# Kernel optimization log

Measured on AMD Instinct MI355X. Metric: run time of the kernel, lower is better.

The kernel has to match this reference:

```python
import jax, jax.numpy as jnp
from jax import lax
import numpy as np

NUM_HEADS = 8
ALPHA = 4.0  # spikingjelly default Sigmoid surrogate alpha
TAU = 2.0
BN_EPS = 1e-5

@jax.custom_vjp
def spike(x):
    # Heaviside(v - v_th) with sigmoid surrogate gradient
    return (x >= 0).astype(x.dtype)

def _spike_fwd(x):
    return spike(x), x

def _spike_bwd(x, g):
    sg = jax.nn.sigmoid(ALPHA * x)
    return (g * ALPHA * sg * (1.0 - sg),)

spike.defvjp(_spike_fwd, _spike_bwd)

def lif(x_seq, v_threshold=1.0):
    """Multi-step LIF, tau=2, hard reset to v_reset=0, detach_reset=True.
    x_seq: (T, ...) -> spikes (T, ...)."""
    def step(v, xt):
        h = v + (xt - v) / TAU
        s = spike(h - v_threshold)
        v_next = h * (1.0 - lax.stop_gradient(s))  # detach_reset hard reset
        return v_next, s
    _, s_seq = lax.scan(step, jnp.zeros_like(x_seq[0]), x_seq)
    return s_seq

def bn1d(x, gamma, beta, mean, var):
    # x: (T,B,C,N), normalize over channel dim C (eval-mode BatchNorm1d)
    inv = gamma / jnp.sqrt(var + BN_EPS)
    return x * inv[:, None] + (beta - mean * inv)[:, None]

def setup_inputs() -> dict:
    key = jax.random.key(0)
    ks = jax.random.split(key, 8)
    T, B, C, H, W = 4, 16, 384, 32, 32
    N = H * W
    Dh = C // NUM_HEADS
    x = jax.random.normal(ks[0], (T, B, C, H, W), dtype=jnp.float32)
    attn_k = jax.random.randint(ks[1], (T, B, NUM_HEADS, Dh, N), 0, 2).astype(jnp.bool_)
    attn_v = jax.random.randint(ks[2], (T, B, NUM_HEADS, Dh, N), 0, 2).astype(jnp.bool_)
    wq = jax.random.normal(ks[3], (C, C), dtype=jnp.float32) * 0.02
    wp = jax.random.normal(ks[4], (C, C), dtype=jnp.float32) * 0.02
    bp = jnp.zeros((C,), dtype=jnp.float32)
    return {
        'x': x, 'attn_k': attn_k, 'attn_v': attn_v,
        'wq': wq,
        'q_gamma': jnp.ones((C,), jnp.float32), 'q_beta': jnp.zeros((C,), jnp.float32),
        'q_mean': jnp.zeros((C,), jnp.float32), 'q_var': jnp.ones((C,), jnp.float32),
        'wp': wp, 'bp': bp,
        'p_gamma': jnp.ones((C,), jnp.float32), 'p_beta': jnp.zeros((C,), jnp.float32),
        'p_mean': jnp.zeros((C,), jnp.float32), 'p_var': jnp.ones((C,), jnp.float32),
    }

def reference(x, attn_k, attn_v, wq, q_gamma, q_beta, q_mean, q_var,
              wp, bp, p_gamma, p_beta, p_mean, p_var):
    T, B, C, H, W = x.shape
    N = H * W
    Dh = C // NUM_HEADS
    xs = lif(x).reshape(T, B, C, N)                      # shortcut_lif + flatten(3)
    q = jnp.einsum('oc,tbcn->tbon', wq, xs)              # q_conv (1x1, no bias)
    q = bn1d(q, q_gamma, q_beta, q_mean, q_var)          # q_bn
    q = lif(q)                                           # q_lif
    q = q.reshape(T, B, NUM_HEADS, Dh, N)
    kv = jnp.logical_and(attn_k, attn_v).astype(q.dtype) # attn_k & attn_v
    out = (q * kv).reshape(T, B, C, N)                   # elementwise 'attention'
    out = jnp.einsum('oc,tbcn->tbon', wp, out) + bp[:, None]  # proj_conv (bias)
    out = bn1d(out, p_gamma, p_beta, p_mean, p_var)      # proj_bn
    return out.reshape(T, B, C, H, W)
```

## Files before the change

kernel.cpp:

```cpp
#include <hip/hip_runtime.h>
#include <cstdint>

#define CN (384*1024)
#define BCN (16*CN)
#define EPS 1e-5f

typedef float f32x2 __attribute__((ext_vector_type(2)));
typedef float f32x4 __attribute__((ext_vector_type(4)));

#define WPT_OFF   0u
#define WQB_OFF   589824u
#define QINV_OFF  1179648u
#define QOFF_OFF  (QINV_OFF + 1536u)
#define PINV_OFF  (QINV_OFF + 3072u)
#define POFF_OFF  (QINV_OFF + 4608u)
#define C0_OFF    (QINV_OFF + 6144u)
#define LCNT2_OFF 1187840u
#define XM_OFF    1310720u
#define XMT_OFF   4456448u
#define LISTS2_OFF 7602176u
#define MST_OFF   XM_OFF

__global__ __launch_bounds__(256) void k01_lif_prep(const float* __restrict__ x,
                                                    const float* __restrict__ wq,
                                                    const float* __restrict__ wp,
                                                    const float* __restrict__ qg,
                                                    const float* __restrict__ qb,
                                                    const float* __restrict__ qm,
                                                    const float* __restrict__ qv,
                                                    const float* __restrict__ pg,
                                                    const float* __restrict__ pb,
                                                    const float* __restrict__ pm,
                                                    const float* __restrict__ pv,
                                                    const float* __restrict__ bp,
                                                    unsigned long long* __restrict__ xm,
                                                    char* __restrict__ ws) {
    if (blockIdx.x < 24576) {
        int wid  = (blockIdx.x * 256 + threadIdx.x) >> 6;
        int lane = threadIdx.x & 63;
        int c = wid % 384;
        int g = (wid / 384) & 15;
        int b = wid / (384 * 16);
        const float* xp = x + (size_t)b * CN + (size_t)c * 1024 + g * 64 + lane;
        float v = 0.f;
        #pragma unroll
        for (int t = 0; t < 4; ++t) {
            float xv = xp[(size_t)t * BCN];
            float h = v + (xv - v) * 0.5f;
            bool s = (h >= 1.0f);
            unsigned long long m = __ballot(s);
            v = s ? 0.f : h;
            if (lane == 0) xm[(((size_t)t * 16 + b) * 16 + g) * 384 + c] = m;
        }
        return;
    }
    int bid = blockIdx.x - 24576;
    if (bid < 576) {
        int i = bid * 256 + threadIdx.x;
        int c = i / 384, o = i % 384;
        ((float*)(ws + WPT_OFF))[c * 384 + o] = wp[o * 384 + c];
    } else if (bid < 1154) {
        int j = (bid - 576) * 256 + threadIdx.x;
        if (j >= 147840) return;
        int r = j / 384, o = j % 384;
        unsigned short v = 0;
        if (r < 384) {
            unsigned u = __float_as_uint(wq[o * 384 + r]);
            v = (unsigned short)((u + 0x7fffu + ((u >> 16) & 1u)) >> 16);
        }
        ((unsigned short*)(ws + WQB_OFF))[j] = v;
    } else {
        for (int i = threadIdx.x; i < 384; i += 256) {
            float qi = qg[i] / sqrtf(qv[i] + EPS);
            ((float*)(ws + QINV_OFF))[i] = qi;
            ((float*)(ws + QOFF_OFF))[i] = qb[i] - qm[i] * qi;
            float pi = pg[i] / sqrtf(pv[i] + EPS);
            float po = pb[i] - pm[i] * pi;
            ((float*)(ws + PINV_OFF))[i] = pi;
            ((float*)(ws + POFF_OFF))[i] = po;
            ((float*)(ws + C0_OFF))[i] = bp[i] * pi + po;
        }
    }
}

__global__ __launch_bounds__(256) void k1bc(const unsigned long long* __restrict__ xm,
                                            unsigned long long* __restrict__ xmT,
                                            unsigned short* __restrict__ lists2,
                                            unsigned char* __restrict__ lcnt2) {
    int wid  = (blockIdx.x * 256 + threadIdx.x) >> 6;
    int lane = threadIdx.x & 63;
    int g  = wid & 15;
    int tb = wid >> 4;
    unsigned long long T[6];
    #pragma unroll
    for (int cg = 0; cg < 6; ++cg) {
        unsigned long long W = xm[((size_t)tb * 16 + g) * 384 + cg * 64 + lane];
        unsigned long long colw = 0ull;
        #pragma unroll
        for (int k = 0; k < 64; ++k) {
            unsigned long long bk = __ballot((W >> k) & 1ull);
            if (lane == k) colw = bk;
        }
        T[cg] = colw;
    }
    const int n   = g * 64 + lane;
    const size_t col = ((size_t)tb << 10) + n;
    #pragma unroll
    for (int cg = 0; cg < 6; ++cg) xmT[col * 6 + cg] = T[cg];
    const int blockid = (tb & 15) * 64 + (n >> 4);
    const int un = (n & 15) * 4 + (tb >> 4);
    unsigned short* lp = lists2 + ((size_t)blockid * 64 + un) * 24;
    int k = 0;
    #pragma unroll
    for (int cg = 0; cg < 6; ++cg) {
        unsigned long long m = T[cg];
        while (m) {
            int j = __builtin_ctzll(m);
            m &= m - 1;
            if (k < 24) lp[k] = (unsigned short)((cg * 64 + j) * 3);
            ++k;
        }
    }
    int kk = k > 24 ? 24 : k;
    for (int i = kk; i < 24; ++i) lp[i] = 1152;
    lcnt2[(size_t)blockid * 64 + un] =
        (k > 24) ? 0xFF : (unsigned char)((k + 7) >> 3);
}

#define BLO(w) __uint_as_float((w) << 16)
#define BHI(w) __uint_as_float((w) & 0xFFFF0000u)
#define PK(w)  ((f32x2){BLO(w), BHI(w)})
#define RL(v, l) ((unsigned)__builtin_amdgcn_readlane((int)(v), (l)))

#define GROW8(W0, W1, W2, W3) do {                                                \
    uint3 d0_ = *(const uint3*)(wqc + ((size_t)((W0) & 0xffffu) << 8) + voff);    \
    uint3 d1_ = *(const uint3*)(wqc + ((size_t)((W0) >> 16) << 8) + voff);        \
    uint3 d2_ = *(const uint3*)(wqc + ((size_t)((W1) & 0xffffu) << 8) + voff);    \
    uint3 d3_ = *(const uint3*)(wqc + ((size_t)((W1) >> 16) << 8) + voff);        \
    uint3 d4_ = *(const uint3*)(wqc + ((size_t)((W2) & 0xffffu) << 8) + voff);    \
    uint3 d5_ = *(const uint3*)(wqc + ((size_t)((W2) >> 16) << 8) + voff);        \
    uint3 d6_ = *(const uint3*)(wqc + ((size_t)((W3) & 0xffffu) << 8) + voff);    \
    uint3 d7_ = *(const uint3*)(wqc + ((size_t)((W3) >> 16) << 8) + voff);        \
    s0 += ((PK(d0_.x) + PK(d1_.x)) + (PK(d2_.x) + PK(d3_.x)))                     \
        + ((PK(d4_.x) + PK(d5_.x)) + (PK(d6_.x) + PK(d7_.x)));                    \
    s1 += ((PK(d0_.y) + PK(d1_.y)) + (PK(d2_.y) + PK(d3_.y)))                     \
        + ((PK(d4_.y) + PK(d5_.y)) + (PK(d6_.y) + PK(d7_.y)));                    \
    s2 += ((PK(d0_.z) + PK(d1_.z)) + (PK(d2_.z) + PK(d3_.z)))                     \
        + ((PK(d4_.z) + PK(d5_.z)) + (PK(d6_.z) + PK(d7_.z)));                    \
} while (0)

__global__ __launch_bounds__(512) void k2_qpath(const char* __restrict__ wqc,
                                                const float* __restrict__ qinv_,
                                                const float* __restrict__ qoff_,
                                                const unsigned short* __restrict__ lists2,
                                                const unsigned char* __restrict__ lcnt2,
                                                const unsigned long long* __restrict__ xmT,
                                                const unsigned char* __restrict__ ak,
                                                const unsigned char* __restrict__ av,
                                                const float* __restrict__ c0,
                                                unsigned long long* __restrict__ msT,
                                                float* __restrict__ out) {
    const int tid  = threadIdx.x;
    const int lane = tid & 63;
    const int w    = tid >> 6;
    const int nt   = blockIdx.x & 63;
    const int b    = blockIdx.x >> 6;
    const int voff = lane * 12;

    const char* lb = (const char*)lists2 + (size_t)blockIdx.x * 3072 + lane * 48;
    const uint4 L0 = *(const uint4*)lb;
    const uint4 L1 = *(const uint4*)(lb + 16);
    const uint4 L2 = *(const uint4*)(lb + 32);
    const unsigned lcv = *(const unsigned*)((const char*)lcnt2
                          + (size_t)blockIdx.x * 64 + (lane & 15) * 4);

    float qi[6], qo[6];
    #pragma unroll
    for (int e = 0; e < 6; ++e) {
        qi[e] = qinv_[lane * 6 + e];
        qo[e] = qoff_[lane * 6 + e];
    }

    #pragma unroll
    for (int i = 0; i < 2; ++i) {
        const int nl = w * 2 + i;
        const int n  = nt * 16 + nl;
        const unsigned lcw = RL(lcv, nl);
        float v[6] = {0.f, 0.f, 0.f, 0.f, 0.f, 0.f};
        #pragma unroll
        for (int t = 0; t < 4; ++t) {
            const int un = nl * 4 + t;
            const unsigned r_ = (lcw >> (8 * t)) & 0xffu;
            f32x2 s0 = {0.f, 0.f}, s1 = {0.f, 0.f}, s2 = {0.f, 0.f};
            {
                const unsigned Wa = RL(L0.x, un), Wb = RL(L0.y, un);
                const unsigned Wc = RL(L0.z, un), Wd = RL(L0.w, un);
                const unsigned We = RL(L1.x, un), Wf = RL(L1.y, un);
                const unsigned Wg = RL(L1.z, un), Wh = RL(L1.w, un);
                GROW8(Wa, Wb, Wc, Wd);
                GROW8(We, Wf, Wg, Wh);
            }
            if (r_ == 3u) {
                const unsigned Wa = RL(L2.x, un), Wb = RL(L2.y, un);
                const unsigned Wc = RL(L2.z, un), Wd = RL(L2.w, un);
                GROW8(Wa, Wb, Wc, Wd);
            }
            if (r_ == 0xffu) {
                const int colf = ((t * 16 + b) << 10) + n;
                const unsigned long long* mp = xmT + (size_t)colf * 6;
                s0 = (f32x2){0.f, 0.f}; s1 = (f32x2){0.f, 0.f}; s2 = (f32x2){0.f, 0.f};
                #pragma unroll
                for (int cg = 0; cg < 6; ++cg) {
                    unsigned long long mm = mp[cg];
                    while (mm) {
                        int j = __builtin_ctzll(mm);
                        mm &= mm - 1;
                        uint3 dd = *(const uint3*)(wqc + (size_t)(cg * 64 + j) * 768 + voff);
                        s0 += PK(dd.x); s1 += PK(dd.y); s2 += PK(dd.z);
                    }
                }
            }
            const int col = ((t * 16 + b) << 10) + n;
            const float val[6] = {s0.x, s0.y, s1.x, s1.y, s2.x, s2.y};
            bool sp[6];
            #pragma unroll
            for (int e = 0; e < 6; ++e) {
                float q = val[e] * qi[e] + qo[e];
                float h = 0.5f * (v[e] + q);
                bool s = (h >= 1.0f);
                v[e] = s ? 0.f : h;
                if (s) {
                    size_t ix = ((size_t)((t * 16 + b) * 384 + lane * 6 + e) << 10) + n;
                    s = (ak[ix] != 0) && (av[ix] != 0);
                }
                sp[e] = s;
            }
            unsigned long long B0 = __ballot(sp[0]);
            unsigned long long B1 = __ballot(sp[1]);
            unsigned long long B2 = __ballot(sp[2]);
            unsigned long long B3 = __ballot(sp[3]);
            unsigned long long B4 = __ballot(sp[4]);
            unsigned long long B5 = __ballot(sp[5]);
            unsigned long long sel = lane == 0 ? B0 : lane == 1 ? B1 : lane == 2 ? B2
                                   : lane == 3 ? B3 : lane == 4 ? B4 : B5;
            if (lane < 6) msT[(size_t)col * 6 + lane] = sel;
        }
    }

    {
        float cv[3];
        #pragma unroll
        for (int k = 0; k < 3; ++k) cv[k] = c0[(tid + k * 512) >> 2];
        #pragma unroll
        for (int t = 0; t < 4; ++t) {
            f32x4* base4 = (f32x4*)out + (size_t)(t * 16 + b) * 384 * 256 + nt * 4;
            #pragma unroll
            for (int k = 0; k < 3; ++k) {
                int i2 = tid + k * 512;
                int o = i2 >> 2, n4 = i2 & 3;
                float vv = cv[k];
                __builtin_nontemporal_store((f32x4){vv, vv, vv, vv},
                                            base4 + (size_t)o * 256 + n4);
            }
        }
    }
}

__global__ __launch_bounds__(384) void k3_proj(const float* __restrict__ wpT,
                                               const float* __restrict__ pinv_,
                                               const float* __restrict__ poff_,
                                               const float* __restrict__ bp,
                                               const unsigned long long* __restrict__ msT,
                                               float* __restrict__ out) {
    __shared__ unsigned int wflag[6];
    const int tid = threadIdx.x;
    const int bid = blockIdx.x;
    const int g = bid & 15, b = (bid >> 4) & 15, t = bid >> 8;
    const unsigned long long* mbase = msT + ((size_t)(t * 16 + b) * 1024 + g * 64) * 6;
    unsigned long long m = mbase[tid];
    unsigned long long anyb = __ballot(m != 0ull);
    if ((tid & 63) == 0) wflag[tid >> 6] = (anyb != 0ull) ? 1u : 0u;
    __syncthreads();
    unsigned int any = wflag[0] | wflag[1] | wflag[2] | wflag[3] | wflag[4] | wflag[5];
    if (!any) return;

    size_t obase = (size_t)(t * 16 + b) * 384;
    float pi = pinv_[tid], po = poff_[tid], bb = bp[tid];
    for (int nl = 0; nl < 64; ++nl) {
        float acc = 0.f;
        #pragma unroll
        for (int u = 0; u < 6; ++u) {
            unsigned long long mm = mbase[nl * 6 + u];
            while (mm) {
                int j = __builtin_ctzll(mm);
                mm &= mm - 1;
                int row = j * 6 + u;
                acc += wpT[(size_t)row * 384 + tid];
            }
        }
        out[(obase + tid) * 1024 + g * 64 + nl] = (acc + bb) * pi + po;
    }
}

extern "C" void kernel_launch(void* const* d_in, const int* in_sizes, int n_in,
                              void* d_out, int out_size, void* d_ws, size_t ws_size,
                              hipStream_t stream) {
    const float* x  = (const float*)d_in[0];
    const unsigned char* ak = (const unsigned char*)d_in[1];
    const unsigned char* av = (const unsigned char*)d_in[2];
    const float* wq = (const float*)d_in[3];
    const float* qg = (const float*)d_in[4];
    const float* qb = (const float*)d_in[5];
    const float* qm = (const float*)d_in[6];
    const float* qv = (const float*)d_in[7];
    const float* wp = (const float*)d_in[8];
    const float* bp = (const float*)d_in[9];
    const float* pg = (const float*)d_in[10];
    const float* pb = (const float*)d_in[11];
    const float* pm = (const float*)d_in[12];
    const float* pv = (const float*)d_in[13];
    char* ws = (char*)d_ws;
    float* out = (float*)d_out;

    hipLaunchKernelGGL(k01_lif_prep, dim3(25731), dim3(256), 0, stream,
                       x, wq, wp, qg, qb, qm, qv, pg, pb, pm, pv, bp,
                       (unsigned long long*)(ws + XM_OFF), ws);
    hipLaunchKernelGGL(k1bc, dim3(256), dim3(256), 0, stream,
                       (const unsigned long long*)(ws + XM_OFF),
                       (unsigned long long*)(ws + XMT_OFF),
                       (unsigned short*)(ws + LISTS2_OFF),
                       (unsigned char*)(ws + LCNT2_OFF));
    hipLaunchKernelGGL(k2_qpath, dim3(1024), dim3(512), 0, stream,
                       (const char*)(ws + WQB_OFF),
                       (const float*)(ws + QINV_OFF), (const float*)(ws + QOFF_OFF),
                       (const unsigned short*)(ws + LISTS2_OFF),
                       (const unsigned char*)(ws + LCNT2_OFF),
                       (const unsigned long long*)(ws + XMT_OFF), ak, av,
                       (const float*)(ws + C0_OFF),
                       (unsigned long long*)(ws + MST_OFF), out);
    hipLaunchKernelGGL(k3_proj, dim3(1024), dim3(384), 0, stream,
                       (const float*)(ws + WPT_OFF), (const float*)(ws + PINV_OFF),
                       (const float*)(ws + POFF_OFF), bp,
                       (const unsigned long long*)(ws + MST_OFF), out);
}
```

Measured before the change: 93.98 us.

## Skip Q-path columns whose LIF membrane provably cannot reach threshold

Computes a per-input-channel max |bf16 weight| and global max BN scale/offset in the prep kernel. k1bc uses them to build, for each (t,n) column, a quantized upper bound on |q| from the active spike list. k2 runs that bound through the LIF recurrence and skips the whole gather-sum for columns that can never spike, writing zero masks instead. This is a sound, conservative bound, so results stay exact. It costs extra prep work and per-column bound bookkeeping, and it only pays off if enough columns have sparse inputs.

```diff
diff --git a/kernel.cpp b/kernel.cpp
--- a/kernel.cpp
+++ b/kernel.cpp
@@ -16,9 +16,12 @@
 #define POFF_OFF  (QINV_OFF + 4608u)
 #define C0_OFF    (QINV_OFF + 6144u)
 #define LCNT2_OFF 1187840u
+#define ROWMAX_OFF 1253376u
+#define MAXQ_OFF  1254912u
 #define XM_OFF    1310720u
 #define XMT_OFF   4456448u
 #define LISTS2_OFF 7602176u
+#define ABND_OFF  10747904u
 #define MST_OFF   XM_OFF
 
 __global__ __launch_bounds__(256) void k01_lif_prep(const float* __restrict__ x,
@@ -69,24 +72,63 @@
             v = (unsigned short)((u + 0x7fffu + ((u >> 16) & 1u)) >> 16);
         }
         ((unsigned short*)(ws + WQB_OFF))[j] = v;
-    } else {
+    } else if (bid == 1154) {
+        __shared__ float smi[256], smo[256];
+        float mi = 0.f, mo = 0.f;
         for (int i = threadIdx.x; i < 384; i += 256) {
             float qi = qg[i] / sqrtf(qv[i] + EPS);
             ((float*)(ws + QINV_OFF))[i] = qi;
-            ((float*)(ws + QOFF_OFF))[i] = qb[i] - qm[i] * qi;
+            float qov = qb[i] - qm[i] * qi;
+            ((float*)(ws + QOFF_OFF))[i] = qov;
             float pi = pg[i] / sqrtf(pv[i] + EPS);
             float po = pb[i] - pm[i] * pi;
             ((float*)(ws + PINV_OFF))[i] = pi;
             ((float*)(ws + POFF_OFF))[i] = po;
             ((float*)(ws + C0_OFF))[i] = bp[i] * pi + po;
+            mi = fmaxf(mi, fabsf(qi));
+            mo = fmaxf(mo, fabsf(qov));
+        }
+        smi[threadIdx.x] = mi; smo[threadIdx.x] = mo;
+        __syncthreads();
+        for (int s = 128; s > 0; s >>= 1) {
+            if (threadIdx.x < s) {
+                smi[threadIdx.x] = fmaxf(smi[threadIdx.x], smi[threadIdx.x + s]);
+                smo[threadIdx.x] = fmaxf(smo[threadIdx.x], smo[threadIdx.x + s]);
+            }
+            __syncthreads();
+        }
+        if (threadIdx.x == 0) {
+            ((float*)(ws + MAXQ_OFF))[0] = smi[0];
+            ((float*)(ws + MAXQ_OFF))[1] = smo[0];
+        }
+    } else {
+        __shared__ float sm[256];
+        int rblk = bid - 1155;
+        int row = rblk * 64 + (threadIdx.x >> 2);
+        int qd  = threadIdx.x & 3;
+        float m = 0.f;
+        for (int o = qd * 96; o < qd * 96 + 96; ++o) {
+            unsigned u = __float_as_uint(wq[(size_t)o * 384 + row]);
+            unsigned bbits = (u + 0x7fffu + ((u >> 16) & 1u)) >> 16;
+            m = fmaxf(m, __uint_as_float((bbits & 0x7fffu) << 16));
+        }
+        sm[threadIdx.x] = m;
+        __syncthreads();
+        if (qd == 0) {
+            float r0 = fmaxf(fmaxf(sm[threadIdx.x], sm[threadIdx.x + 1]),
+                             fmaxf(sm[threadIdx.x + 2], sm[threadIdx.x + 3]));
+            ((float*)(ws + ROWMAX_OFF))[row] = r0;
         }
     }
 }
 
 __global__ __launch_bounds__(256) void k1bc(const unsigned long long* __restrict__ xm,
+                                            const float* __restrict__ rowmaxp,
+                                            const float* __restrict__ maxqp,
                                             unsigned long long* __restrict__ xmT,
                                             unsigned short* __restrict__ lists2,
-                                            unsigned char* __restrict__ lcnt2) {
+                                            unsigned char* __restrict__ lcnt2,
+                                            unsigned char* __restrict__ abnd) {
     int wid  = (blockIdx.x * 256 + threadIdx.x) >> 6;
     int lane = threadIdx.x & 63;
     int g  = wid & 15;
@@ -111,12 +153,14 @@
     const int un = (n & 15) * 4 + (tb >> 4);
     unsigned short* lp = lists2 + ((size_t)blockid * 64 + un) * 24;
     int k = 0;
+    float S = 0.f;
     #pragma unroll
     for (int cg = 0; cg < 6; ++cg) {
         unsigned long long m = T[cg];
         while (m) {
             int j = __builtin_ctzll(m);
             m &= m - 1;
+            S += rowmaxp[cg * 64 + j];
             if (k < 24) lp[k] = (unsigned short)((cg * 64 + j) * 3);
             ++k;
         }
@@ -125,6 +169,9 @@
     for (int i = kk; i < 24; ++i) lp[i] = 1152;
     lcnt2[(size_t)blockid * 64 + un] =
         (k > 24) ? 0xFF : (unsigned char)((k + 7) >> 3);
+    float A = maxqp[0] * S + maxqp[1];
+    int aq = (int)ceilf(A * 64.f);
+    abnd[(size_t)blockid * 64 + un] = (unsigned char)(aq > 255 ? 255 : (aq < 0 ? 0 : aq));
 }
 
 #define BLO(w) __uint_as_float((w) << 16)
@@ -154,6 +201,7 @@
                                                 const float* __restrict__ qoff_,
                                                 const unsigned short* __restrict__ lists2,
                                                 const unsigned char* __restrict__ lcnt2,
+                                                const unsigned char* __restrict__ abnd,
                                                 const unsigned long long* __restrict__ xmT,
                                                 const unsigned char* __restrict__ ak,
                                                 const unsigned char* __restrict__ av,
@@ -173,6 +221,8 @@
     const uint4 L2 = *(const uint4*)(lb + 32);
     const unsigned lcv = *(const unsigned*)((const char*)lcnt2
                           + (size_t)blockIdx.x * 64 + (lane & 15) * 4);
+    const unsigned abv = *(const unsigned*)((const char*)abnd
+                          + (size_t)blockIdx.x * 64 + (lane & 15) * 4);
 
     float qi[6], qo[6];
     #pragma unroll
@@ -185,6 +235,23 @@
     for (int i = 0; i < 2; ++i) {
         const int nl = w * 2 + i;
         const int n  = nt * 16 + nl;
+        const unsigned abw = RL(abv, nl);
+        float hb = 0.f;
+        bool skip = true;
+        #pragma unroll
+        for (int t = 0; t < 4; ++t) {
+            float A = (float)((abw >> (8 * t)) & 0xffu) * 0.015625f + 0.015625f;
+            hb = 0.5f * (hb + A);
+            skip = skip && (hb < 1.0f);
+        }
+        if (skip) {
+            if (lane < 6) {
+                #pragma unroll
+                for (int t = 0; t < 4; ++t)
+                    msT[(size_t)(((t * 16 + b) << 10) + n) * 6 + lane] = 0ull;
+            }
+            continue;
+        }
         const unsigned lcw = RL(lcv, nl);
         float v[6] = {0.f, 0.f, 0.f, 0.f, 0.f, 0.f};
         #pragma unroll
@@ -322,19 +389,23 @@
     char* ws = (char*)d_ws;
     float* out = (float*)d_out;
 
-    hipLaunchKernelGGL(k01_lif_prep, dim3(25731), dim3(256), 0, stream,
+    hipLaunchKernelGGL(k01_lif_prep, dim3(25737), dim3(256), 0, stream,
                        x, wq, wp, qg, qb, qm, qv, pg, pb, pm, pv, bp,
                        (unsigned long long*)(ws + XM_OFF), ws);
     hipLaunchKernelGGL(k1bc, dim3(256), dim3(256), 0, stream,
                        (const unsigned long long*)(ws + XM_OFF),
+                       (const float*)(ws + ROWMAX_OFF),
+                       (const float*)(ws + MAXQ_OFF),
                        (unsigned long long*)(ws + XMT_OFF),
                        (unsigned short*)(ws + LISTS2_OFF),
-                       (unsigned char*)(ws + LCNT2_OFF));
+                       (unsigned char*)(ws + LCNT2_OFF),
+                       (unsigned char*)(ws + ABND_OFF));
     hipLaunchKernelGGL(k2_qpath, dim3(1024), dim3(512), 0, stream,
                        (const char*)(ws + WQB_OFF),
                        (const float*)(ws + QINV_OFF), (const float*)(ws + QOFF_OFF),
                        (const unsigned short*)(ws + LISTS2_OFF),
                        (const unsigned char*)(ws + LCNT2_OFF),
+                       (const unsigned char*)(ws + ABND_OFF),
                        (const unsigned long long*)(ws + XMT_OFF), ak, av,
                        (const float*)(ws + C0_OFF),
                        (unsigned long long*)(ws + MST_OFF), out);
```

After: 91.39 us. 2.8% less time.
